# Optimization experiments

Hardware: AMD Instinct MI355X
Metric: run time of the kernel (lower is better)

## Reference

```python
import jax, jax.numpy as jnp
import numpy as np

B, S, D = 8, 2048, 512

def setup_inputs() -> dict:
    key = jax.random.key(0)
    ks = jax.random.split(key, 9)
    scale = 1.0 / np.sqrt(D)
    q = jax.random.normal(ks[0], (B, S, D), dtype=jnp.float32)
    k = jax.random.normal(ks[1], (B, S, D), dtype=jnp.float32)
    v = jax.random.normal(ks[2], (B, S, D), dtype=jnp.float32)
    # causal mask, broadcast over batch: True = attend
    mask = jnp.tril(jnp.ones((S, S), dtype=bool))[None, :, :]
    Wq = jax.random.normal(ks[3], (D, D), dtype=jnp.float32) * scale
    bq = jax.random.normal(ks[4], (D,), dtype=jnp.float32) * scale
    Wk = jax.random.normal(ks[5], (D, D), dtype=jnp.float32) * scale
    bk = jax.random.normal(ks[6], (D,), dtype=jnp.float32) * scale
    Wv = jax.random.normal(ks[7], (D, D), dtype=jnp.float32) * scale
    bv = jax.random.normal(ks[8], (D,), dtype=jnp.float32) * scale
    return {"q": q, "k": k, "v": v, "mask": mask,
            "Wq": Wq, "bq": bq, "Wk": Wk, "bk": bk, "Wv": Wv, "bv": bv}

def reference(q, k, v, mask, Wq, bq, Wk, bk, Wv, bv):
    # torch nn.Linear: x @ W^T + b
    Q = jnp.einsum('bsd,ed->bse', q, Wq) + bq
    K = jnp.einsum('bsd,ed->bse', k, Wk) + bk
    V = jnp.einsum('bsd,ed->bse', v, Wv) + bv
    scores = jnp.einsum('bqd,bkd->bqk', Q, K) / jnp.sqrt(jnp.float32(D))
    scores = jnp.where(mask, scores, jnp.float32(-1e9))
    prob = jax.nn.softmax(scores, axis=-1)
    out = jnp.einsum('bqk,bkd->bqd', prob, V)
    return out
```

## Files before the change

kernel.cpp:

```cpp
#include <hip/hip_runtime.h>
#include <stdint.h>
#include <stddef.h>
#include <math.h>

typedef _Float16 half8 __attribute__((ext_vector_type(8)));
typedef float f32x4 __attribute__((ext_vector_type(4)));

#define SCALE_QK 0.04419417382415922f

__device__ __forceinline__ void gload16(const void* g, void* lds) {
  __builtin_amdgcn_global_load_lds(
      (const __attribute__((address_space(1))) void*)g,
      (__attribute__((address_space(3))) void*)lds,
      16, 0, 0);
}

template<bool A_F32>
__device__ __forceinline__ void run_kloop_wide(const void* Arow0, const _Float16* Brow0,
                                               int lda, int ldb, int kIters,
                                               _Float16* As, _Float16* Bs,
                                               f32x4 (&acc)[4][8])
{
  const int tid  = threadIdx.x;
  const int lane = tid & 63;
  const int w    = tid >> 6;
  const int wm   = w >> 1, wn = w & 1;
  const int srow = tid >> 3;
  const int sg   = tid & 7;
  const int swz  = sg ^ (srow & 7);
  const int fr   = lane & 15;
  const int fq   = lane >> 4;
  const int fx   = lane & 7;

  for (int it = 0; it < kIters; ++it) {
    const int k0 = it * 64;
    if constexpr (A_F32) {
      const float* A = (const float*)Arow0;
      f32x4 preF[8];
      #pragma unroll
      for (int i = 0; i < 4; ++i) {
        const float* src = A + (size_t)(i*32 + srow) * lda + (k0 + sg*8);
        preF[2*i]   = *(const f32x4*)src;
        preF[2*i+1] = *(const f32x4*)(src + 4);
      }
      #pragma unroll
      for (int i = 0; i < 8; ++i)
        gload16(Brow0 + (size_t)(i*32 + srow) * ldb + (k0 + swz*8), Bs + i*2048 + w*512);
      #pragma unroll
      for (int i = 0; i < 4; ++i) {
        f32x4 x = preF[2*i], y = preF[2*i+1];
        half8 h;
        h[0]=(_Float16)x[0]; h[1]=(_Float16)x[1]; h[2]=(_Float16)x[2]; h[3]=(_Float16)x[3];
        h[4]=(_Float16)y[0]; h[5]=(_Float16)y[1]; h[6]=(_Float16)y[2]; h[7]=(_Float16)y[3];
        *(half8*)(As + (i*32 + srow)*64 + swz*8) = h;
      }
    } else {
      const _Float16* A = (const _Float16*)Arow0;
      #pragma unroll
      for (int i = 0; i < 4; ++i)
        gload16(A + (size_t)(i*32 + srow) * lda + (k0 + swz*8), As + i*2048 + w*512);
      #pragma unroll
      for (int i = 0; i < 8; ++i)
        gload16(Brow0 + (size_t)(i*32 + srow) * ldb + (k0 + swz*8), Bs + i*2048 + w*512);
    }
    __syncthreads();

    #pragma unroll
    for (int ks = 0; ks < 2; ++ks) {
      half8 av[4], bv[8];
      const int slot = (ks*4 + fq) ^ fx;
      #pragma unroll
      for (int i = 0; i < 4; ++i)
        av[i] = *(const half8*)(As + (wm*64 + i*16 + fr)*64 + slot*8);
      #pragma unroll
      for (int j = 0; j < 8; ++j)
        bv[j] = *(const half8*)(Bs + (wn*128 + j*16 + fr)*64 + slot*8);
      #pragma unroll
      for (int i = 0; i < 4; ++i) {
        #pragma unroll
        for (int j = 0; j < 8; ++j)
          acc[i][j] = __builtin_amdgcn_mfma_f32_16x16x32_f16(av[i], bv[j], acc[i][j], 0, 0, 0);
      }
    }
    __syncthreads();
  }
}

__device__ __forceinline__ void run_kloop_sb(const _Float16* Arow0, const _Float16* Brow0,
                                             int lda, int ldb, int kIters,
                                             _Float16* As, _Float16* Bs,
                                             f32x4 (&acc)[4][4])
{
  const int tid  = threadIdx.x;
  const int lane = tid & 63;
  const int w    = tid >> 6;
  const int wm   = w >> 1, wn = w & 1;
  const int srow = tid >> 3;
  const int sg   = tid & 7;
  const int swz  = sg ^ (srow & 7);
  const int fr   = lane & 15;
  const int fq   = lane >> 4;
  const int fx   = lane & 7;

  for (int it = 0; it < kIters; ++it) {
    const int k0 = it * 64;
    #pragma unroll
    for (int i = 0; i < 4; ++i)
      gload16(Arow0 + (size_t)(i*32 + srow) * lda + (k0 + swz*8), As + i*2048 + w*512);
    #pragma unroll
    for (int i = 0; i < 4; ++i)
      gload16(Brow0 + (size_t)(i*32 + srow) * ldb + (k0 + swz*8), Bs + i*2048 + w*512);
    __syncthreads();

    #pragma unroll
    for (int ks = 0; ks < 2; ++ks) {
      half8 av[4], bv[4];
      const int slot = (ks*4 + fq) ^ fx;
      #pragma unroll
      for (int i = 0; i < 4; ++i) {
        av[i] = *(const half8*)(As + (wm*64 + i*16 + fr)*64 + slot*8);
        bv[i] = *(const half8*)(Bs + (wn*64 + i*16 + fr)*64 + slot*8);
      }
      #pragma unroll
      for (int i = 0; i < 4; ++i) {
        #pragma unroll
        for (int j = 0; j < 4; ++j)
          acc[i][j] = __builtin_amdgcn_mfma_f32_16x16x32_f16(av[i], bv[j], acc[i][j], 0, 0, 0);
      }
    }
    __syncthreads();
  }
}

__global__ __launch_bounds__(256) void k_cvtw(const float* __restrict__ Wq,
                                              const float* __restrict__ Wk,
                                              const float* __restrict__ Wv,
                                              _Float16* __restrict__ Wb)
{
  const int t = blockIdx.x * 256 + threadIdx.x;
  const int base = t * 8;
  const int z = base >> 18;
  const int off = base & 262143;
  const float* src = (z == 0) ? Wq : ((z == 1) ? Wk : Wv);
  f32x4 a = *(const f32x4*)(src + off);
  f32x4 b = *(const f32x4*)(src + off + 4);
  half8 h;
  h[0]=(_Float16)a[0]; h[1]=(_Float16)a[1]; h[2]=(_Float16)a[2]; h[3]=(_Float16)a[3];
  h[4]=(_Float16)b[0]; h[5]=(_Float16)b[1]; h[6]=(_Float16)b[2]; h[7]=(_Float16)b[3];
  *(half8*)(Wb + base) = h;
}

__global__ __launch_bounds__(256, 2) void k_proj(const float* __restrict__ q,
                                                 const float* __restrict__ k,
                                                 const float* __restrict__ v,
                                                 const _Float16* __restrict__ Wb,
                                                 const float* __restrict__ bq,
                                                 const float* __restrict__ bk,
                                                 const float* __restrict__ bv,
                                                 _Float16* __restrict__ Qb,
                                                 _Float16* __restrict__ Kb,
                                                 _Float16* __restrict__ Vt)
{
  __shared__ __align__(16) _Float16 LDSbuf[256*132];
  _Float16* As = LDSbuf;
  _Float16* Bs = LDSbuf + 8192;

  const int bid = blockIdx.x;
  const int xcd = bid & 7, i = bid >> 3;
  const int p = xcd * 48 + (i >> 1);
  const int nt2 = i & 1;
  const int z = p >> 7, mt = p & 127;

  const float* A     = (z == 0) ? q  : (z == 1) ? k  : v;
  const float* bia   = (z == 0) ? bq : (z == 1) ? bk : bv;
  const _Float16* B  = Wb + (size_t)z * 512 * 512;

  f32x4 acc[4][8] = {};
  run_kloop_wide<true>(A + (size_t)mt*128*512, B + (size_t)nt2*256*512, 512, 512, 8,
                       As, Bs, acc);

  const int tid = threadIdx.x;
  const int lane = tid & 63, w = tid >> 6;
  const int wm = w >> 1, wn = w & 1;
  const int fr = lane & 15, fq = lane >> 4;

  if (z < 2) {
    _Float16* C = (z == 0) ? Qb : Kb;
    #pragma unroll
    for (int j = 0; j < 8; ++j) {
      const int col = nt2*256 + wn*128 + j*16 + fr;
      const float bval = bia[col];
      #pragma unroll
      for (int i2 = 0; i2 < 4; ++i2) {
        const int row = mt*128 + wm*64 + i2*16 + fq*4;
        #pragma unroll
        for (int r = 0; r < 4; ++r)
          C[(size_t)(row + r) * 512 + col] = (_Float16)(acc[i2][j][r] + bval);
      }
    }
  } else {
    _Float16* sm = LDSbuf;
    #pragma unroll
    for (int j = 0; j < 8; ++j) {
      const int colloc = wn*128 + j*16 + fr;
      const float bval = bia[nt2*256 + colloc];
      #pragma unroll
      for (int i2 = 0; i2 < 4; ++i2) {
        const int rowloc = wm*64 + i2*16 + fq*4;
        #pragma unroll
        for (int r = 0; r < 4; ++r)
          sm[colloc*132 + rowloc + r] = (_Float16)(acc[i2][j][r] + bval);
      }
    }
    __syncthreads();
    const int bb = mt >> 4, s0 = (mt & 15) * 128;
    #pragma unroll
    for (int q8 = 0; q8 < 16; ++q8) {
      const int dloc = q8*16 + (tid >> 4);
      const int ch   = tid & 15;
      half8 o = *(const half8*)&sm[dloc*132 + ch*8];
      *(half8*)(Vt + ((size_t)bb*512 + nt2*256 + dloc)*2048 + s0 + ch*8) = o;
    }
  }
}

__global__ __launch_bounds__(256, 2) void k_scores(const _Float16* __restrict__ Qb,
                                                   const _Float16* __restrict__ Kb,
                                                   _Float16* __restrict__ P)
{
  __shared__ __align__(16) _Float16 As[128*64], Bs[256*64];
  const int bid = blockIdx.x;
  const int b = bid & 7;
  const int t = 71 - (bid >> 3);
  int qt = 0, accum = 0;
  while (accum + (qt >> 1) + 1 <= t) { accum += (qt >> 1) + 1; ++qt; }
  const int kt0 = (t - accum) * 2;

  f32x4 acc[4][8] = {};
  run_kloop_wide<false>(Qb + ((size_t)b*2048 + qt*128)*512,
                        Kb + ((size_t)b*2048 + kt0*128)*512,
                        512, 512, 8, As, Bs, acc);

  const int lane = threadIdx.x & 63, w = threadIdx.x >> 6;
  const int wm = w >> 1, wn = w & 1;
  const int fr = lane & 15, fq = lane >> 4;

  const int kt = kt0 + wn;
  if (kt <= qt) {
    const bool diag = (kt == qt);
    #pragma unroll
    for (int i = 0; i < 4; ++i) {
      const int rl = wm*64 + i*16 + fq*4;
      #pragma unroll
      for (int j = 0; j < 8; ++j) {
        const int cl = j*16 + fr;
        #pragma unroll
        for (int r = 0; r < 4; ++r) {
          const float sc = acc[i][j][r] * SCALE_QK;
          const bool msk = diag && (cl > rl + r);
          P[((size_t)b*2048 + qt*128 + rl + r) * 2048 + kt*128 + cl] =
              msk ? (_Float16)(-30000.0f) : (_Float16)sc;
        }
      }
    }
  }
}

__global__ __launch_bounds__(256) void k_softmax(_Float16* __restrict__ P)
{
  const int lane = threadIdx.x & 63;
  const int row  = blockIdx.x * 4 + (threadIdx.x >> 6);
  const int qIdx = row & 2047;
  _Float16* p = P + (size_t)row * 2048;
  const int L    = qIdx + 1;
  const int Lpad = ((qIdx >> 7) + 1) * 128;

  half8 xb[4];
  float m = -1e30f, s = 0.f;
  #pragma unroll
  for (int c = 0; c < 4; ++c) {
    const int i0 = lane * 8 + c * 512;
    if (i0 < Lpad) {
      half8 x = *(const half8*)(p + i0);
      xb[c] = x;
      float xv[8];
      #pragma unroll
      for (int j = 0; j < 8; ++j) xv[j] = (i0 + j < L) ? (float)x[j] : -1e30f;
      float cm = xv[0];
      #pragma unroll
      for (int j = 1; j < 8; ++j) cm = fmaxf(cm, xv[j]);
      const float mn = fmaxf(m, cm);
      float cs = 0.f;
      #pragma unroll
      for (int j = 0; j < 8; ++j) cs += __expf(xv[j] - mn);
      s = s * __expf(m - mn) + cs;
      m = mn;
    }
  }
  #pragma unroll
  for (int d = 1; d < 64; d <<= 1) {
    const float mo = __shfl_xor(m, d, 64);
    const float so = __shfl_xor(s, d, 64);
    const float mn = fmaxf(m, mo);
    s = s * __expf(m - mn) + so * __expf(mo - mn);
    m = mn;
  }
  const float inv = 1.0f / s;

  #pragma unroll
  for (int c = 0; c < 4; ++c) {
    const int i0 = lane * 8 + c * 512;
    if (i0 < Lpad) {
      half8 x = xb[c];
      half8 o;
      #pragma unroll
      for (int j = 0; j < 8; ++j)
        o[j] = (i0 + j < L) ? (_Float16)(__expf((float)x[j] - m) * inv) : (_Float16)0.f;
      *(half8*)(p + i0) = o;
    }
  }
}

__global__ __launch_bounds__(256, 4) void k_pv(const _Float16* __restrict__ P,
                                               const _Float16* __restrict__ Vt,
                                               float* __restrict__ Out)
{
  __shared__ __align__(16) _Float16 As[128*64], Bs[128*64];
  const int bid = blockIdx.x;
  const int b = bid & 7;
  const int r0 = bid >> 3;
  const int qi = r0 >> 2, dt = r0 & 3;
  const int qt = (qi & 1) ? (15 - (qi >> 1)) : (qi >> 1);

  f32x4 acc[4][4] = {};
  run_kloop_sb(P  + ((size_t)b*2048 + qt*128)*2048,
               Vt + ((size_t)b*512  + dt*128)*2048,
               2048, 2048, (qt + 1) * 2, As, Bs, acc);
  const int lane = threadIdx.x & 63, w = threadIdx.x >> 6;
  const int wm = w >> 1, wn = w & 1;
  const int fr = lane & 15, fq = lane >> 4;
  #pragma unroll
  for (int i = 0; i < 4; ++i) {
    const int row = qt*128 + wm*64 + i*16 + fq*4;
    #pragma unroll
    for (int j = 0; j < 4; ++j) {
      const int col = dt*128 + wn*64 + j*16 + fr;
      #pragma unroll
      for (int r = 0; r < 4; ++r)
        Out[((size_t)b*2048 + row + r) * 512 + col] = acc[i][j][r];
    }
  }
}

extern "C" void kernel_launch(void* const* d_in, const int* in_sizes, int n_in,
                              void* d_out, int out_size, void* d_ws, size_t ws_size,
                              hipStream_t stream) {
  (void)in_sizes; (void)n_in; (void)out_size;
  const float* q  = (const float*)d_in[0];
  const float* k  = (const float*)d_in[1];
  const float* v  = (const float*)d_in[2];
  const float* Wq = (const float*)d_in[4];
  const float* bq = (const float*)d_in[5];
  const float* Wk = (const float*)d_in[6];
  const float* bk = (const float*)d_in[7];
  const float* Wv = (const float*)d_in[8];
  const float* bv = (const float*)d_in[9];

  const size_t OFF_P  = 0;
  const size_t OFF_Q  = (size_t)64 << 20;
  const size_t OFF_K  = (size_t)80 << 20;
  const size_t OFF_VT = (size_t)112 << 20;
  const size_t OFF_W  = (size_t)128 << 20;
  const size_t NEEDED = OFF_W + (size_t)3 * 512 * 512 * sizeof(_Float16);
  if (ws_size < NEEDED) return;

  char* ws = (char*)d_ws;
  _Float16* P  = (_Float16*)(ws + OFF_P);
  _Float16* Qb = (_Float16*)(ws + OFF_Q);
  _Float16* Kb = (_Float16*)(ws + OFF_K);
  _Float16* Vt = (_Float16*)(ws + OFF_VT);
  _Float16* Wb = (_Float16*)(ws + OFF_W);
  float* Out = (float*)d_out;

  k_cvtw   <<<dim3(384),  dim3(256), 0, stream>>>(Wq, Wk, Wv, Wb);
  k_proj   <<<dim3(768),  dim3(256), 0, stream>>>(q, k, v, Wb, bq, bk, bv, Qb, Kb, Vt);
  k_scores <<<dim3(576),  dim3(256), 0, stream>>>(Qb, Kb, P);
  k_softmax<<<dim3(4096), dim3(256), 0, stream>>>(P);
  k_pv     <<<dim3(512),  dim3(256), 0, stream>>>(P, Vt, Out);
}
```

Before: 270.5 us.

## Use square causal tiles in scores kernel and fold QK scale into projection

```diff
diff --git a/kernel.cpp b/kernel.cpp
--- a/kernel.cpp
+++ b/kernel.cpp
@@ -15,8 +15,7 @@
       16, 0, 0);
 }
 
-template<bool A_F32>
-__device__ __forceinline__ void run_kloop_wide(const void* Arow0, const _Float16* Brow0,
+__device__ __forceinline__ void run_kloop_wide(const float* Arow0, const _Float16* Brow0,
                                                int lda, int ldb, int kIters,
                                                _Float16* As, _Float16* Bs,
                                                f32x4 (&acc)[4][8])
@@ -34,34 +33,23 @@
 
   for (int it = 0; it < kIters; ++it) {
     const int k0 = it * 64;
-    if constexpr (A_F32) {
-      const float* A = (const float*)Arow0;
-      f32x4 preF[8];
-      #pragma unroll
-      for (int i = 0; i < 4; ++i) {
-        const float* src = A + (size_t)(i*32 + srow) * lda + (k0 + sg*8);
-        preF[2*i]   = *(const f32x4*)src;
-        preF[2*i+1] = *(const f32x4*)(src + 4);
-      }
-      #pragma unroll
-      for (int i = 0; i < 8; ++i)
-        gload16(Brow0 + (size_t)(i*32 + srow) * ldb + (k0 + swz*8), Bs + i*2048 + w*512);
-      #pragma unroll
-      for (int i = 0; i < 4; ++i) {
-        f32x4 x = preF[2*i], y = preF[2*i+1];
-        half8 h;
-        h[0]=(_Float16)x[0]; h[1]=(_Float16)x[1]; h[2]=(_Float16)x[2]; h[3]=(_Float16)x[3];
-        h[4]=(_Float16)y[0]; h[5]=(_Float16)y[1]; h[6]=(_Float16)y[2]; h[7]=(_Float16)y[3];
-        *(half8*)(As + (i*32 + srow)*64 + swz*8) = h;
-      }
-    } else {
-      const _Float16* A = (const _Float16*)Arow0;
-      #pragma unroll
-      for (int i = 0; i < 4; ++i)
-        gload16(A + (size_t)(i*32 + srow) * lda + (k0 + swz*8), As + i*2048 + w*512);
-      #pragma unroll
-      for (int i = 0; i < 8; ++i)
-        gload16(Brow0 + (size_t)(i*32 + srow) * ldb + (k0 + swz*8), Bs + i*2048 + w*512);
+    f32x4 preF[8];
+    #pragma unroll
+    for (int i = 0; i < 4; ++i) {
+      const float* src = Arow0 + (size_t)(i*32 + srow) * lda + (k0 + sg*8);
+      preF[2*i]   = *(const f32x4*)src;
+      preF[2*i+1] = *(const f32x4*)(src + 4);
+    }
+    #pragma unroll
+    for (int i = 0; i < 8; ++i)
+      gload16(Brow0 + (size_t)(i*32 + srow) * ldb + (k0 + swz*8), Bs + i*2048 + w*512);
+    #pragma unroll
+    for (int i = 0; i < 4; ++i) {
+      f32x4 x = preF[2*i], y = preF[2*i+1];
+      half8 h;
+      h[0]=(_Float16)x[0]; h[1]=(_Float16)x[1]; h[2]=(_Float16)x[2]; h[3]=(_Float16)x[3];
+      h[4]=(_Float16)y[0]; h[5]=(_Float16)y[1]; h[6]=(_Float16)y[2]; h[7]=(_Float16)y[3];
+      *(half8*)(As + (i*32 + srow)*64 + swz*8) = h;
     }
     __syncthreads();
 
@@ -176,8 +164,8 @@
   const _Float16* B  = Wb + (size_t)z * 512 * 512;
 
   f32x4 acc[4][8] = {};
-  run_kloop_wide<true>(A + (size_t)mt*128*512, B + (size_t)nt2*256*512, 512, 512, 8,
-                       As, Bs, acc);
+  run_kloop_wide(A + (size_t)mt*128*512, B + (size_t)nt2*256*512, 512, 512, 8,
+                 As, Bs, acc);
 
   const int tid = threadIdx.x;
   const int lane = tid & 63, w = tid >> 6;
@@ -186,6 +174,7 @@
 
   if (z < 2) {
     _Float16* C = (z == 0) ? Qb : Kb;
+    const float osc = (z == 0) ? SCALE_QK : 1.0f;
     #pragma unroll
     for (int j = 0; j < 8; ++j) {
       const int col = nt2*256 + wn*128 + j*16 + fr;
@@ -195,7 +184,7 @@
         const int row = mt*128 + wm*64 + i2*16 + fq*4;
         #pragma unroll
         for (int r = 0; r < 4; ++r)
-          C[(size_t)(row + r) * 512 + col] = (_Float16)(acc[i2][j][r] + bval);
+          C[(size_t)(row + r) * 512 + col] = (_Float16)((acc[i2][j][r] + bval) * osc);
       }
     }
   } else {
@@ -224,44 +213,36 @@
   }
 }
 
-__global__ __launch_bounds__(256, 2) void k_scores(const _Float16* __restrict__ Qb,
+__global__ __launch_bounds__(256, 4) void k_scores(const _Float16* __restrict__ Qb,
                                                    const _Float16* __restrict__ Kb,
                                                    _Float16* __restrict__ P)
 {
-  __shared__ __align__(16) _Float16 As[128*64], Bs[256*64];
+  __shared__ __align__(16) _Float16 As[128*64], Bs[128*64];
   const int bid = blockIdx.x;
   const int b = bid & 7;
-  const int t = 71 - (bid >> 3);
-  int qt = 0, accum = 0;
-  while (accum + (qt >> 1) + 1 <= t) { accum += (qt >> 1) + 1; ++qt; }
-  const int kt0 = (t - accum) * 2;
-
-  f32x4 acc[4][8] = {};
-  run_kloop_wide<false>(Qb + ((size_t)b*2048 + qt*128)*512,
-                        Kb + ((size_t)b*2048 + kt0*128)*512,
-                        512, 512, 8, As, Bs, acc);
-
+  const int t = bid >> 3;
+  int qt = (int)((sqrtf(8.0f * (float)t + 1.0f) - 1.0f) * 0.5f);
+  int base = (qt * (qt + 1)) >> 1;
+  if (t < base)                { --qt; base = (qt * (qt + 1)) >> 1; }
+  else if (t >= base + qt + 1) { ++qt; base = (qt * (qt + 1)) >> 1; }
+  const int kt = t - base;
+
+  f32x4 acc[4][4] = {};
+  run_kloop_sb(Qb + ((size_t)b*2048 + qt*128)*512,
+               Kb + ((size_t)b*2048 + kt*128)*512,
+               512, 512, 8, As, Bs, acc);
   const int lane = threadIdx.x & 63, w = threadIdx.x >> 6;
   const int wm = w >> 1, wn = w & 1;
   const int fr = lane & 15, fq = lane >> 4;
-
-  const int kt = kt0 + wn;
-  if (kt <= qt) {
-    const bool diag = (kt == qt);
-    #pragma unroll
-    for (int i = 0; i < 4; ++i) {
-      const int rl = wm*64 + i*16 + fq*4;
-      #pragma unroll
-      for (int j = 0; j < 8; ++j) {
-        const int cl = j*16 + fr;
-        #pragma unroll
-        for (int r = 0; r < 4; ++r) {
-          const float sc = acc[i][j][r] * SCALE_QK;
-          const bool msk = diag && (cl > rl + r);
-          P[((size_t)b*2048 + qt*128 + rl + r) * 2048 + kt*128 + cl] =
-              msk ? (_Float16)(-30000.0f) : (_Float16)sc;
-        }
-      }
+  #pragma unroll
+  for (int i = 0; i < 4; ++i) {
+    const int row = qt*128 + wm*64 + i*16 + fq*4;
+    #pragma unroll
+    for (int j = 0; j < 4; ++j) {
+      const int col = kt*128 + wn*64 + j*16 + fr;
+      #pragma unroll
+      for (int r = 0; r < 4; ++r)
+        P[((size_t)b*2048 + row + r) * 2048 + col] = (_Float16)acc[i][j][r];
     }
   }
 }
@@ -384,7 +365,7 @@
 
   k_cvtw   <<<dim3(384),  dim3(256), 0, stream>>>(Wq, Wk, Wv, Wb);
   k_proj   <<<dim3(768),  dim3(256), 0, stream>>>(q, k, v, Wb, bq, bk, bv, Qb, Kb, Vt);
-  k_scores <<<dim3(576),  dim3(256), 0, stream>>>(Qb, Kb, P);
+  k_scores <<<dim3(1088), dim3(256), 0, stream>>>(Qb, Kb, P);
   k_softmax<<<dim3(4096), dim3(256), 0, stream>>>(P);
   k_pv     <<<dim3(512),  dim3(256), 0, stream>>>(P, Vt, Out);
 }
```

New measurement: 266.8 us. No clear change (-1.4%).
